# Kernel optimization log

Measured on AMD Instinct MI355X. Metric: run time of the kernel, lower is better.

The kernel has to match this reference:

```python
import jax, jax.numpy as jnp
import numpy as np


def setup_inputs() -> dict:
    key = jax.random.key(0)
    k0, k1, k2, k3, k4 = jax.random.split(key, 5)
    dim, b, h, w = 256, 32, 56, 56
    x = jax.random.normal(k0, (b, dim, h, w), jnp.float32)
    # 1x1 conv qk: weight [out=dim, in=dim], bias [dim]
    qk_w = jax.random.normal(k1, (dim, dim), jnp.float32) * (1.0 / np.sqrt(dim))
    qk_b = jax.random.normal(k2, (dim,), jnp.float32) * 0.01
    # depthwise 3x3 conv pe: weight [dim, 1, 3, 3], bias [dim]
    pe_w = jax.random.normal(k3, (dim, 1, 3, 3), jnp.float32) * (1.0 / 3.0)
    pe_b = jax.random.normal(k4, (dim,), jnp.float32) * 0.01
    return {"x": x, "qk_w": qk_w, "qk_b": qk_b, "pe_w": pe_w, "pe_b": pe_b}


def reference(x, qk_w, qk_b, pe_w, pe_b):
    b, c, h, w = x.shape
    n = h * w
    d = c // 2                      # head_dim = dim // 2
    s = float(n) ** -0.5
    # 1x1 conv + (elu + 1) feature map
    qk = jnp.einsum('bchw,oc->bohw', x, qk_w) + qk_b[None, :, None, None]
    qk = jax.nn.elu(qk) + 1.0
    qk = qk.reshape(b, 2, d, n)
    q, k = qk[:, 0], qk[:, 1]       # each [b, d, n]
    v = x.reshape(b, c, n)          # [b, c, n]
    # kv outer product: (k*s) @ (v^T * s) -> [b, d, c]
    kv = jnp.einsum('bdn,bcn->bdc', k, v) * (s * s)
    # numerator q^T @ kv -> [b, n, c]
    num = jnp.einsum('bdn,bdc->bnc', q, kv)
    # denominator q^T @ mean(k, axis=-1) -> [b, n, 1]
    den = jnp.einsum('bdn,bd->bn', q, jnp.mean(k, axis=-1))[:, :, None] + 1e-6
    attn = (num / den).transpose(0, 2, 1).reshape(b, c, h, w)
    # depthwise 3x3 positional conv on v (= x)
    pe = jax.lax.conv_general_dilated(
        x, pe_w, window_strides=(1, 1), padding='SAME',
        dimension_numbers=('NCHW', 'OIHW', 'NCHW'), feature_group_count=c)
    return attn + pe + pe_b[None, :, None, None]
```

## Files before the change

### kernel.cpp

```cpp
#include <hip/hip_runtime.h>

#define B_ 32
#define C_ 256
#define D_ 128
#define HH 56
#define WW 56
#define N_ 3136
#define KSPLIT 7
#define KRANGE 448

typedef float f32x4 __attribute__((ext_vector_type(4)));
typedef short s16x8 __attribute__((ext_vector_type(8)));
typedef unsigned short u16x8 __attribute__((ext_vector_type(8)));

__device__ __forceinline__ int swz4(int r){
  return (r & 3) ^ (((r >> 2) & 1) << 1) ^ ((r >> 3) & 1);
}
__device__ __forceinline__ unsigned short f2bf(float f){
  unsigned u = __float_as_uint(f);
  u += 0x7fffu + ((u >> 16) & 1u);
  return (unsigned short)(u >> 16);
}
__device__ __forceinline__ float bf2f(unsigned short h){
  return __uint_as_float(((unsigned)h) << 16);
}
__device__ __forceinline__ float elu1(float v){
  return v > 0.f ? v + 1.f : __expf(v);
}
__device__ __forceinline__ unsigned cvtpk(float lo, float hi){
  unsigned r;
  asm("v_cvt_pk_bf16_f32 %0, %1, %2" : "=v"(r) : "v"(lo), "v"(hi));
  return r;
}

template<int R>
__device__ __forceinline__ void stage_glds(const unsigned short* gp, int ld, char* lds){
  const int tid = threadIdx.x;
  const int wid = tid >> 6;
#pragma unroll
  for (int q = 0; q < R/64; ++q){
    const int slot = q*256 + tid;
    const int r = slot >> 2, gi = slot & 3;
    const int u = gi ^ swz4(r);
    const unsigned short* ga = gp + r*ld + u*8;
    char* lb = lds + (q*256 + wid*64)*16;
    __builtin_amdgcn_global_load_lds(
        (__attribute__((address_space(1))) void*)ga,
        (__attribute__((address_space(3))) void*)lb, 16, 0, 0);
  }
}

__device__ __forceinline__ s16x8 ldsfrag(const char* lds, int r, int g){
  return *(const s16x8*)(lds + r*64 + ((g ^ swz4(r)) << 4));
}

__global__ __launch_bounds__(256) void k0_w(
    const float* __restrict__ w, unsigned short* __restrict__ wb)
{
  const int i = blockIdx.x*256 + threadIdx.x;
  float4 v = *(const float4*)(w + (size_t)i*4);
  uint2 h = {cvtpk(v.x, v.y), cvtpk(v.z, v.w)};
  *(uint2*)(wb + (size_t)i*4) = h;
}

__global__ __launch_bounds__(256) void k1_qk(
    const float* __restrict__ x, const unsigned short* __restrict__ wb,
    const float* __restrict__ bias,
    unsigned short* __restrict__ kbuf, unsigned short* __restrict__ qt)
{
  __shared__ __align__(16) char Al[256*64];
  __shared__ __align__(16) char Bl[64*64];
  const int tid = threadIdx.x, lane = tid & 63, wid = tid >> 6;
  const int n0 = blockIdx.x * 64;
  const int b  = blockIdx.y;
  const float* xb = x + (size_t)b*C_*N_;
  const int wo = wid*64;
  f32x4 acc[4][4] = {};

  for (int k0 = 0; k0 < C_; k0 += 32){
    float4 xv[2];
    int cc[2], nn[2];
#pragma unroll
    for (int q = 0; q < 2; ++q){
      const int idx = q*256 + tid;
      cc[q] = idx >> 4;
      nn[q] = (idx & 15)*4;
      xv[q] = *(const float4*)(xb + (size_t)(k0 + cc[q])*N_ + n0 + nn[q]);
    }
    __syncthreads();
    stage_glds<256>(wb + k0, C_, Al);
#pragma unroll
    for (int q = 0; q < 2; ++q){
      const float vv[4] = {xv[q].x, xv[q].y, xv[q].z, xv[q].w};
#pragma unroll
      for (int i = 0; i < 4; ++i){
        const int r = nn[q] + i;
        *(unsigned short*)(Bl + r*64 + ((cc[q]*2) ^ (swz4(r) << 4))) = f2bf(vv[i]);
      }
    }
    __syncthreads();
    s16x8 af[4], bv4[4];
#pragma unroll
    for (int m = 0; m < 4; ++m)  af[m]  = ldsfrag(Al, wo + m*16 + (lane & 15), lane >> 4);
#pragma unroll
    for (int nf = 0; nf < 4; ++nf) bv4[nf] = ldsfrag(Bl, nf*16 + (lane & 15), lane >> 4);
#pragma unroll
    for (int m = 0; m < 4; ++m)
#pragma unroll
      for (int nf = 0; nf < 4; ++nf)
        acc[m][nf] = __builtin_amdgcn_mfma_f32_16x16x32_bf16(af[m], bv4[nf], acc[m][nf], 0, 0, 0);
  }

  const int col = lane & 15, rg = lane >> 4;
  if (wid < 2){
#pragma unroll
    for (int m = 0; m < 4; ++m){
      const int db = wo + m*16 + rg*4;
      const float b0 = bias[db], b1 = bias[db+1], b2 = bias[db+2], b3 = bias[db+3];
#pragma unroll
      for (int nf = 0; nf < 4; ++nf){
        const int n = n0 + nf*16 + col;
        f32x4 a = acc[m][nf];
        uint2 hv = {cvtpk(elu1(a[0]+b0), elu1(a[1]+b1)),
                    cvtpk(elu1(a[2]+b2), elu1(a[3]+b3))};
        *(uint2*)(qt + ((size_t)b*N_ + n)*D_ + db) = hv;
      }
    }
  } else {
#pragma unroll
    for (int m = 0; m < 4; ++m)
#pragma unroll
      for (int j = 0; j < 4; ++j){
        const int d = wo - 128 + m*16 + rg*4 + j;
        const float bb = bias[128 + d];
#pragma unroll
        for (int nf = 0; nf < 4; ++nf){
          const int n = n0 + nf*16 + col;
          kbuf[((size_t)b*D_ + d)*N_ + n] = f2bf(elu1(acc[m][nf][j] + bb));
        }
      }
  }
}

__global__ __launch_bounds__(512) void k2_kv(
    const unsigned short* __restrict__ kbuf, const float* __restrict__ x,
    unsigned short* __restrict__ kvp, float* __restrict__ kmp)
{
  __shared__ __align__(16) char Al[128*64];
  __shared__ __align__(16) char Bl[256*64];
  const int tid = threadIdx.x, lane = tid & 63, wid = tid >> 6;
  const int ks = blockIdx.x;
  const int b  = blockIdx.y;
  const unsigned short* kb = kbuf + (size_t)b*D_*N_ + ks*KRANGE;
  const float* xb = x + (size_t)b*C_*N_ + ks*KRANGE;
  const int wd = (wid >> 2)*64, wc = (wid & 3)*64;
  f32x4 acc[4][4] = {};
  float kms = 0.f;
  const int sr = tid >> 2, sg = tid & 3;

  for (int t = 0; t < KRANGE/32; ++t){
    __syncthreads();
    {
      const int u = sg ^ swz4(sr);
      const unsigned short* ga = kb + (size_t)sr*N_ + t*32 + u*8;
      char* lb = Al + (wid*64)*16;
      __builtin_amdgcn_global_load_lds(
          (__attribute__((address_space(1))) void*)ga,
          (__attribute__((address_space(3))) void*)lb, 16, 0, 0);
    }
#pragma unroll
    for (int q = 0; q < 4; ++q){
      int idx = q*512 + tid;
      int cc = idx >> 3, n4 = (idx & 7)*4;
      float4 v = *(const float4*)(xb + (size_t)cc*N_ + t*32 + n4);
      uint2 h = {cvtpk(v.x, v.y), cvtpk(v.z, v.w)};
      *(uint2*)(Bl + cc*64 + ((n4*2) ^ (swz4(cc) << 4))) = h;
    }
    __syncthreads();
    s16x8 af[4], bv[4];
#pragma unroll
    for (int m = 0; m < 4; ++m)  af[m] = ldsfrag(Al, wd + m*16 + (lane & 15), lane >> 4);
#pragma unroll
    for (int cf = 0; cf < 4; ++cf) bv[cf] = ldsfrag(Bl, wc + cf*16 + (lane & 15), lane >> 4);
#pragma unroll
    for (int m = 0; m < 4; ++m)
#pragma unroll
      for (int cf = 0; cf < 4; ++cf)
        acc[m][cf] = __builtin_amdgcn_mfma_f32_16x16x32_bf16(af[m], bv[cf], acc[m][cf], 0, 0, 0);
    {
      uint2 u = *(const uint2*)(Al + sr*64 + ((sg ^ swz4(sr)) << 4));
      uint2 u2 = *(const uint2*)(Al + sr*64 + ((sg ^ swz4(sr)) << 4) + 8);
      const unsigned ua[4] = {u.x, u.y, u2.x, u2.y};
#pragma unroll
      for (int i = 0; i < 4; ++i){
        kms += bf2f((unsigned short)(ua[i] & 0xffffu));
        kms += bf2f((unsigned short)(ua[i] >> 16));
      }
    }
  }

  kms += __shfl_xor(kms, 1);
  kms += __shfl_xor(kms, 2);
  if ((tid & 3) == 0) kmp[((size_t)b*KSPLIT + ks)*D_ + sr] = kms;

  const int col = lane & 15, rg = lane >> 4;
#pragma unroll
  for (int m = 0; m < 4; ++m){
    const int d0 = wd + m*16 + rg*4;
#pragma unroll
    for (int cf = 0; cf < 4; ++cf){
      const int c = wc + cf*16 + col;
      ushort4 hv = {f2bf(acc[m][cf][0]), f2bf(acc[m][cf][1]),
                    f2bf(acc[m][cf][2]), f2bf(acc[m][cf][3])};
      *(ushort4*)(kvp + (((size_t)b*KSPLIT + ks)*C_ + c)*D_ + d0) = hv;
    }
  }
}

__global__ __launch_bounds__(256) void kr_reduce(
    const unsigned short* __restrict__ kvp, const float* __restrict__ kmp,
    unsigned short* __restrict__ kvt, float* __restrict__ km)
{
  const int tid = threadIdx.x;
  const int bx = blockIdx.x, b = blockIdx.y;
  const float sc = 1.0f/(float)N_;
#pragma unroll
  for (int it = 0; it < 2; ++it){
    const int idx = (bx*2 + it)*256 + tid;
    const int c = idx >> 4, dq = (idx & 15)*8;
    float s[8] = {};
    for (int ks = 0; ks < KSPLIT; ++ks){
      u16x8 v = *(const u16x8*)(kvp + (((size_t)b*KSPLIT + ks)*C_ + c)*D_ + dq);
#pragma unroll
      for (int i = 0; i < 8; ++i) s[i] += bf2f(v[i]);
    }
    u16x8 h;
#pragma unroll
    for (int i = 0; i < 8; ++i) h[i] = f2bf(s[i]*sc);
    *(u16x8*)(kvt + ((size_t)b*C_ + c)*D_ + dq) = h;
  }
  if (bx == 0 && tid < D_){
    float s = 0.f;
    for (int ks = 0; ks < KSPLIT; ++ks) s += kmp[((size_t)b*KSPLIT + ks)*D_ + tid];
    km[b*D_ + tid] = s*sc;
  }
}

__global__ __launch_bounds__(256) void k3_attn(
    const unsigned short* __restrict__ qt, const unsigned short* __restrict__ kvt,
    const float* __restrict__ km, unsigned short* __restrict__ attn)
{
  __shared__ __align__(16) char SM[256*64 + 64*64];
  char* Al = SM;
  char* Bl = SM + 256*64;
  unsigned short* P = (unsigned short*)SM;
  __shared__ float kms[128];
  __shared__ float dens[64];
  const int tid = threadIdx.x, lane = tid & 63, wid = tid >> 6;
  const int n0 = blockIdx.x * 64;
  const int b  = blockIdx.y;
  if (tid < 128) kms[tid] = km[b*D_ + tid];
  const unsigned short* kvb = kvt + (size_t)b*C_*D_;
  const unsigned short* qtb = qt + ((size_t)b*N_ + n0)*D_;
  const int wc = wid*64;
  f32x4 acc[4][4] = {};
  float den = 0.f;

  for (int k0 = 0; k0 < D_; k0 += 32){
    __syncthreads();
    stage_glds<256>(kvb + k0, D_, Al);
    stage_glds<64>(qtb + k0, D_, Bl);
    __syncthreads();
    s16x8 af[4], bv4[4];
#pragma unroll
    for (int m = 0; m < 4; ++m)  af[m]  = ldsfrag(Al, wc + m*16 + (lane & 15), lane >> 4);
#pragma unroll
    for (int nf = 0; nf < 4; ++nf) bv4[nf] = ldsfrag(Bl, nf*16 + (lane & 15), lane >> 4);
#pragma unroll
    for (int m = 0; m < 4; ++m)
#pragma unroll
      for (int nf = 0; nf < 4; ++nf)
        acc[m][nf] = __builtin_amdgcn_mfma_f32_16x16x32_bf16(af[m], bv4[nf], acc[m][nf], 0, 0, 0);
    {
      const int nr = tid >> 2, g = tid & 3;
      uint4 u = *(const uint4*)(Bl + nr*64 + ((g ^ swz4(nr)) << 4));
      const float* kp = kms + k0 + g*8;
      const unsigned ua[4] = {u.x, u.y, u.z, u.w};
#pragma unroll
      for (int i = 0; i < 4; ++i){
        den += bf2f((unsigned short)(ua[i] & 0xffffu)) * kp[i*2];
        den += bf2f((unsigned short)(ua[i] >> 16))     * kp[i*2 + 1];
      }
    }
  }
  den += __shfl_xor(den, 1);
  den += __shfl_xor(den, 2);
  if ((tid & 3) == 0) dens[tid >> 2] = den;
  __syncthreads();

  const int col = lane & 15, rg = lane >> 4;
  float rdv[4];
#pragma unroll
  for (int nf = 0; nf < 4; ++nf)
    rdv[nf] = 1.0f / (dens[nf*16 + col] + 1e-6f);

#pragma unroll
  for (int h = 0; h < 2; ++h){
    if ((wid >> 1) == h){
      const int lc = wc - h*128;
#pragma unroll
      for (int m = 0; m < 4; ++m)
#pragma unroll
        for (int nf = 0; nf < 4; ++nf)
#pragma unroll
          for (int j = 0; j < 4; ++j)
            P[(lc + m*16 + rg*4 + j)*72 + (nf*16 + col)] = f2bf(acc[m][nf][j] * rdv[nf]);
    }
    __syncthreads();
#pragma unroll
    for (int p = 0; p < 4; ++p){
      const int c = (tid >> 3) + p*32, ch = tid & 7;
      u16x8 v = *(const u16x8*)(P + c*72 + ch*8);
      *(u16x8*)(attn + ((size_t)b*C_ + h*128 + c)*N_ + n0 + ch*8) = v;
    }
    __syncthreads();
  }
}

__global__ __launch_bounds__(256) void k4_pe(
    const float* __restrict__ x, const unsigned short* __restrict__ attn,
    const float* __restrict__ pw, const float* __restrict__ pb,
    float* __restrict__ out)
{
  __shared__ float xs_raw[58*56 + 8];
  float* xs = xs_raw + 4;
  const int tid = threadIdx.x;
  const int ch = blockIdx.x, b = blockIdx.y;
  if (tid < 14)      ((float4*)xs)[tid] = (float4){0.f,0.f,0.f,0.f};
  else if (tid < 28) ((float4*)xs)[784 + tid] = (float4){0.f,0.f,0.f,0.f};
  const float* xp = x + ((size_t)b*C_ + ch)*N_;
  for (int i = tid; i < 784; i += 256)
    ((float4*)xs)[14 + i] = ((const float4*)xp)[i];
  const float* wp = pw + ch*9;
  float wgt[9];
#pragma unroll
  for (int i = 0; i < 9; ++i) wgt[i] = wp[i];
  const float bias = pb[ch];
  __syncthreads();
  const unsigned short* ap = attn + ((size_t)b*C_ + ch)*N_;
  float* op = out + ((size_t)b*C_ + ch)*N_;
  for (int u = tid; u < 784; u += 256) {
    const int row = u / 14, g = u - row*14;
    float o0 = bias, o1 = bias, o2 = bias, o3 = bias;
#pragma unroll
    for (int rr = 0; rr < 3; ++rr){
      const float* rp = xs + (row + rr)*56 + g*4;
      float4 cv = *(const float4*)rp;
      float lf = (g > 0)  ? rp[-1] : 0.f;
      float rt = (g < 13) ? rp[4]  : 0.f;
      const float wl = wgt[rr*3], wc_ = wgt[rr*3+1], wr = wgt[rr*3+2];
      o0 += wl*lf   + wc_*cv.x + wr*cv.y;
      o1 += wl*cv.x + wc_*cv.y + wr*cv.z;
      o2 += wl*cv.y + wc_*cv.z + wr*cv.w;
      o3 += wl*cv.z + wc_*cv.w + wr*rt;
    }
    ushort4 av = *(const ushort4*)(ap + u*4);
    float4 ov = {o0 + bf2f(av.x), o1 + bf2f(av.y), o2 + bf2f(av.z), o3 + bf2f(av.w)};
    *(float4*)(op + u*4) = ov;
  }
}

extern "C" void kernel_launch(void* const* d_in, const int* in_sizes, int n_in,
                              void* d_out, int out_size, void* d_ws, size_t ws_size,
                              hipStream_t stream) {
  (void)in_sizes; (void)n_in; (void)out_size; (void)ws_size;
  const float* x   = (const float*)d_in[0];
  const float* qkw = (const float*)d_in[1];
  const float* qkb = (const float*)d_in[2];
  const float* pew = (const float*)d_in[3];
  const float* peb = (const float*)d_in[4];
  float* out = (float*)d_out;

  unsigned short* slot0 = (unsigned short*)d_ws;
  unsigned short* kbuf = slot0 + (size_t)B_*N_*C_;
  unsigned short* qt   = kbuf + (size_t)B_*D_*N_;
  unsigned short* kvt  = qt   + (size_t)B_*N_*D_;
  float* km  = (float*)(kvt + (size_t)B_*C_*D_);
  unsigned short* wb   = kvt;
  unsigned short* kvp  = slot0;
  float* kmp = (float*)(kvp + (size_t)B_*KSPLIT*C_*D_);
  unsigned short* attn = slot0;

  k0_w     <<<dim3(64),          256, 0, stream>>>(qkw, wb);
  k1_qk    <<<dim3(N_/64, B_),   256, 0, stream>>>(x, wb, qkb, kbuf, qt);
  k2_kv    <<<dim3(KSPLIT, B_),  512, 0, stream>>>(kbuf, x, kvp, kmp);
  kr_reduce<<<dim3(8, B_),       256, 0, stream>>>(kvp, kmp, kvt, km);
  k3_attn  <<<dim3(N_/64, B_),   256, 0, stream>>>(qt, kvt, km, attn);
  k4_pe    <<<dim3(C_, B_),      256, 0, stream>>>(x, attn, pew, peb, out);
}
```

Baseline: 153.3 us.

## Load qk GEMM operands directly from global memory into MFMA fragments, dropping LDS staging

```diff
diff --git a/kernel.cpp b/kernel.cpp
--- a/kernel.cpp
+++ b/kernel.cpp
@@ -68,50 +68,48 @@
     const float* __restrict__ bias,
     unsigned short* __restrict__ kbuf, unsigned short* __restrict__ qt)
 {
-  __shared__ __align__(16) char Al[256*64];
-  __shared__ __align__(16) char Bl[64*64];
   const int tid = threadIdx.x, lane = tid & 63, wid = tid >> 6;
   const int n0 = blockIdx.x * 64;
   const int b  = blockIdx.y;
+  const int col = lane & 15, kg = lane >> 4;
   const float* xb = x + (size_t)b*C_*N_;
   const int wo = wid*64;
   f32x4 acc[4][4] = {};
 
+  const unsigned short* wp[4];
+#pragma unroll
+  for (int m = 0; m < 4; ++m)
+    wp[m] = wb + (size_t)(wo + m*16 + col)*C_ + kg*8;
+  const float* xp[4];
+#pragma unroll
+  for (int nf = 0; nf < 4; ++nf)
+    xp[nf] = xb + (size_t)(kg*8)*N_ + n0 + nf*16 + col;
+
   for (int k0 = 0; k0 < C_; k0 += 32){
-    float4 xv[2];
-    int cc[2], nn[2];
-#pragma unroll
-    for (int q = 0; q < 2; ++q){
-      const int idx = q*256 + tid;
-      cc[q] = idx >> 4;
-      nn[q] = (idx & 15)*4;
-      xv[q] = *(const float4*)(xb + (size_t)(k0 + cc[q])*N_ + n0 + nn[q]);
-    }
-    __syncthreads();
-    stage_glds<256>(wb + k0, C_, Al);
-#pragma unroll
-    for (int q = 0; q < 2; ++q){
-      const float vv[4] = {xv[q].x, xv[q].y, xv[q].z, xv[q].w};
-#pragma unroll
-      for (int i = 0; i < 4; ++i){
-        const int r = nn[q] + i;
-        *(unsigned short*)(Bl + r*64 + ((cc[q]*2) ^ (swz4(r) << 4))) = f2bf(vv[i]);
-      }
-    }
-    __syncthreads();
-    s16x8 af[4], bv4[4];
-#pragma unroll
-    for (int m = 0; m < 4; ++m)  af[m]  = ldsfrag(Al, wo + m*16 + (lane & 15), lane >> 4);
-#pragma unroll
-    for (int nf = 0; nf < 4; ++nf) bv4[nf] = ldsfrag(Bl, nf*16 + (lane & 15), lane >> 4);
+    s16x8 af[4];
+#pragma unroll
+    for (int m = 0; m < 4; ++m)
+      af[m] = *(const s16x8*)(wp[m] + k0);
+    s16x8 bf[4];
+#pragma unroll
+    for (int nf = 0; nf < 4; ++nf){
+      float v[8];
+#pragma unroll
+      for (int j = 0; j < 8; ++j)
+        v[j] = xp[nf][(size_t)(k0 + j)*N_];
+      union { uint4 u; s16x8 s; } pk;
+      pk.u = (uint4){cvtpk(v[0],v[1]), cvtpk(v[2],v[3]),
+                     cvtpk(v[4],v[5]), cvtpk(v[6],v[7])};
+      bf[nf] = pk.s;
+    }
 #pragma unroll
     for (int m = 0; m < 4; ++m)
 #pragma unroll
       for (int nf = 0; nf < 4; ++nf)
-        acc[m][nf] = __builtin_amdgcn_mfma_f32_16x16x32_bf16(af[m], bv4[nf], acc[m][nf], 0, 0, 0);
-  }
-
-  const int col = lane & 15, rg = lane >> 4;
+        acc[m][nf] = __builtin_amdgcn_mfma_f32_16x16x32_bf16(af[m], bf[nf], acc[m][nf], 0, 0, 0);
+  }
+
+  const int rg = lane >> 4;
   if (wid < 2){
 #pragma unroll
     for (int m = 0; m < 4; ++m){
```

Result: slower. 164.7 us (+7.4%).
